# Kernel tuning notes

Measured on AMD Instinct MI355X. Metric: run time of the kernel, lower is better.

Reference implementation:

```python
import jax, jax.numpy as jnp
import numpy as np

N = 4096  # seq len, used for cos/sin positional reweighting


def _non_neg(x):
    # exp(x) for x<0, x+1 for x>=0
    return jnp.where(x < 0, jnp.exp(x), x + 1.0)


def setup_inputs() -> dict:
    key = jax.random.key(0)
    kq, kk, kv = jax.random.split(key, 3)
    shape = (4, 16, N, 64)
    q = jax.random.normal(kq, shape, dtype=jnp.float32)
    k = jax.random.normal(kk, shape, dtype=jnp.float32)
    v = jax.random.normal(kv, shape, dtype=jnp.float32)
    return {"q": q, "k": k, "v": v}


def reference(q, k, v):
    s = q.shape[-2]
    pos = (jnp.pi / 2.0 / s) * jnp.arange(s, dtype=q.dtype)
    cos = jnp.cos(pos)[:, None]  # [S, 1], broadcasts over feature dim
    sin = jnp.sin(pos)[:, None]
    qf = _non_neg(q)
    kf = _non_neg(k)
    q_cos, q_sin = qf * cos, qf * sin  # [B, H, S, D]
    k_cos, k_sin = kf * cos, kf * sin
    # O(N) kv aggregation: [B, H, D, Dv]
    kv_cos = jnp.einsum('bhsd,bhse->bhde', k_cos, v)
    kv_sin = jnp.einsum('bhsd,bhse->bhde', k_sin, v)
    out = jnp.einsum('bhsd,bhde->bhse', q_cos, kv_cos) + \
          jnp.einsum('bhsd,bhde->bhse', q_sin, kv_sin)
    return out
```

## Files before the change

### kernel.cpp

```cpp
#include <hip/hip_runtime.h>
#include <math.h>

#define SLEN 4096
#define DH   64
#define BHN  64
#define CH   8
#define ROWSPER 512
#define SPAD 72

typedef float  f32x4  __attribute__((ext_vector_type(4)));
typedef __bf16 bf16x8 __attribute__((ext_vector_type(8)));

static constexpr float ANG = 1.5707963267948966f / 4096.0f;

static __device__ __forceinline__ float featf(float x) {
    return x < 0.f ? __expf(x) : x + 1.f;
}
static __device__ __forceinline__ void pack2(short* p, float a, float b) {
    union { __bf16 h[2]; unsigned u; } uu;
    uu.h[0] = (__bf16)a; uu.h[1] = (__bf16)b;
    *(unsigned*)p = uu.u;
}

__global__ __launch_bounds__(256) void kv_partial(const float* __restrict__ k,
                                                  const float* __restrict__ v,
                                                  float* __restrict__ part)
{
    __shared__ short kcT[64 * SPAD];
    __shared__ short ksT[64 * SPAD];
    __shared__ short vT [64 * SPAD];

    const int bx = blockIdx.x;
    const int bh = bx >> 3, ch = bx & 7;
    const size_t base = (size_t)bh * SLEN * DH;
    const int t  = threadIdx.x;
    const int wv = t >> 6;
    const int ln = t & 63;
    const int m  = ln & 15;
    const int g  = ln >> 4;

    const int d0 = (t & 15) * 4;
    const int sg = t >> 4;

    f32x4 aC[4] = {}; f32x4 aS[4] = {};

    for (int tile = 0; tile < 8; ++tile) {
        const int srow0 = ch * ROWSPER + tile * 64;
        __syncthreads();
        #pragma unroll
        for (int it = 0; it < 2; ++it) {
            const int sl = it * 32 + sg * 2;
            const int srow = srow0 + sl;
            float sn0, c0, sn1, c1;
            __sincosf(ANG * (float)srow,       &sn0, &c0);
            __sincosf(ANG * (float)(srow + 1), &sn1, &c1);
            const f32x4 k0 = *(const f32x4*)&k[base + (size_t)srow * DH + d0];
            const f32x4 k1 = *(const f32x4*)&k[base + (size_t)(srow + 1) * DH + d0];
            const f32x4 v0 = *(const f32x4*)&v[base + (size_t)srow * DH + d0];
            const f32x4 v1 = *(const f32x4*)&v[base + (size_t)(srow + 1) * DH + d0];
            #pragma unroll
            for (int i = 0; i < 4; ++i) {
                const float kf0 = featf(k0[i]);
                const float kf1 = featf(k1[i]);
                const int rowoff = (d0 + i) * SPAD + sl;
                pack2(&kcT[rowoff], kf0 * c0,  kf1 * c1);
                pack2(&ksT[rowoff], kf0 * sn0, kf1 * sn1);
                pack2(&vT [rowoff], v0[i],     v1[i]);
            }
        }
        __syncthreads();
        #pragma unroll
        for (int b = 0; b < 2; ++b) {
            const int so = b * 32 + g * 8;
            const bf16x8 Ac = *(const bf16x8*)&kcT[(wv * 16 + m) * SPAD + so];
            const bf16x8 As = *(const bf16x8*)&ksT[(wv * 16 + m) * SPAD + so];
            #pragma unroll
            for (int nt = 0; nt < 4; ++nt) {
                const bf16x8 Bv = *(const bf16x8*)&vT[(nt * 16 + m) * SPAD + so];
                aC[nt] = __builtin_amdgcn_mfma_f32_16x16x32_bf16(Ac, Bv, aC[nt], 0, 0, 0);
                aS[nt] = __builtin_amdgcn_mfma_f32_16x16x32_bf16(As, Bv, aS[nt], 0, 0, 0);
            }
        }
    }

    const size_t pb = (size_t)bx * 8192;
    #pragma unroll
    for (int nt = 0; nt < 4; ++nt) {
        #pragma unroll
        for (int r = 0; r < 4; ++r) {
            const size_t rowb = (size_t)(wv * 16 + g * 4 + r) * 64 + nt * 16 + m;
            part[pb        + rowb] = aC[nt][r];
            part[pb + 4096 + rowb] = aS[nt][r];
        }
    }
}

__global__ __launch_bounds__(256) void kv_reduce(const float* __restrict__ part,
                                                 short* __restrict__ kvT)
{
    const int bx = blockIdx.x;
    const int bh = bx >> 2, qd = bx & 3;
    const size_t pbase = (size_t)bh * CH * 8192;
    for (int i = threadIdx.x; i < 2048; i += 256) {
        const int cs = i >> 10;
        const int dl = (i >> 6) & 15;
        const int e  = i & 63;
        const int d  = qd * 16 + dl;
        const int j  = cs * 4096 + d * 64 + e;
        float s = 0.f;
        #pragma unroll
        for (int c = 0; c < CH; ++c) s += part[pbase + (size_t)c * 8192 + j];
        __bf16 hv = (__bf16)s;
        kvT[(size_t)bh * 8192 + cs * 4096 + e * 64 + d] = *(short*)&hv;
    }
}

__global__ __launch_bounds__(256) void out_kernel(const float* __restrict__ q,
                                                  const short* __restrict__ kvT,
                                                  float* __restrict__ out)
{
    const int bx = blockIdx.x;
    const int bh = bx >> 4, chunk = bx & 15;
    const int t = threadIdx.x;
    const int wv = t >> 6, ln = t & 63, m = ln & 15, g = ln >> 4;
    const size_t qbase = (size_t)bh * SLEN * DH;
    const size_t kvb   = (size_t)bh * 8192;

    bf16x8 Bc[4][2], Bs[4][2];
    #pragma unroll
    for (int nt = 0; nt < 4; ++nt)
        #pragma unroll
        for (int b = 0; b < 2; ++b) {
            const int off = (nt * 16 + m) * 64 + b * 32 + g * 8;
            Bc[nt][b] = *(const bf16x8*)&kvT[kvb + off];
            Bs[nt][b] = *(const bf16x8*)&kvT[kvb + 4096 + off];
        }

    const int sA = chunk * 256 + wv * 16 + m;
    f32x4 qb[4], qn[4];
    #pragma unroll
    for (int p = 0; p < 4; ++p)
        qb[p] = *(const f32x4*)&q[qbase + (size_t)sA * DH + (p >> 1) * 32 + g * 8 + (p & 1) * 4];

    for (int it = 0; it < 4; ++it) {
        const int srow = sA + it * 64;
        if (it < 3) {
            #pragma unroll
            for (int p = 0; p < 4; ++p)
                qn[p] = *(const f32x4*)&q[qbase + (size_t)(srow + 64) * DH + (p >> 1) * 32 + g * 8 + (p & 1) * 4];
        }
        float sn, c;
        __sincosf(ANG * (float)srow, &sn, &c);
        union { bf16x8 v; __bf16 e[8]; } Ac[2], As[2];
        #pragma unroll
        for (int p = 0; p < 4; ++p) {
            #pragma unroll
            for (int i = 0; i < 4; ++i) {
                const float qf = featf(qb[p][i]);
                Ac[p >> 1].e[(p & 1) * 4 + i] = (__bf16)(qf * c);
                As[p >> 1].e[(p & 1) * 4 + i] = (__bf16)(qf * sn);
            }
        }
        f32x4 acc[4] = {};
        #pragma unroll
        for (int nt = 0; nt < 4; ++nt) {
            acc[nt] = __builtin_amdgcn_mfma_f32_16x16x32_bf16(Ac[0].v, Bc[nt][0], acc[nt], 0, 0, 0);
            acc[nt] = __builtin_amdgcn_mfma_f32_16x16x32_bf16(Ac[1].v, Bc[nt][1], acc[nt], 0, 0, 0);
            acc[nt] = __builtin_amdgcn_mfma_f32_16x16x32_bf16(As[0].v, Bs[nt][0], acc[nt], 0, 0, 0);
            acc[nt] = __builtin_amdgcn_mfma_f32_16x16x32_bf16(As[1].v, Bs[nt][1], acc[nt], 0, 0, 0);
        }
        const int s0 = chunk * 256 + (it * 4 + wv) * 16;
        #pragma unroll
        for (int r = 0; r < 4; ++r) {
            const size_t ob = ((size_t)bh * SLEN + s0 + g * 4 + r) * 64;
            #pragma unroll
            for (int nt = 0; nt < 4; ++nt)
                out[ob + nt * 16 + m] = acc[nt][r];
        }
        if (it < 3) {
            #pragma unroll
            for (int p = 0; p < 4; ++p) qb[p] = qn[p];
        }
    }
}

extern "C" void kernel_launch(void* const* d_in, const int* in_sizes, int n_in,
                              void* d_out, int out_size, void* d_ws, size_t ws_size,
                              hipStream_t stream) {
    const float* q = (const float*)d_in[0];
    const float* k = (const float*)d_in[1];
    const float* v = (const float*)d_in[2];
    float* out  = (float*)d_out;
    float* part = (float*)d_ws;
    short* kvT  = (short*)((char*)d_ws + (size_t)BHN * CH * 8192 * 4);

    hipLaunchKernelGGL(kv_partial, dim3(BHN * CH), dim3(256), 0, stream, k, v, part);
    hipLaunchKernelGGL(kv_reduce,  dim3(BHN * 4),  dim3(256), 0, stream, part, kvT);
    hipLaunchKernelGGL(out_kernel, dim3(BHN * 16), dim3(256), 0, stream, q, kvT, out);
}
```

Measured before the change: 74.40 us.

## Pipeline kv_partial loads, swizzle LDS, rotate sincos, store bf16 partials

kv_partial now splits each sequence into 16 chunks of 256 rows instead of 8 of 512. It double-buffers the global K/V loads in registers so the next tile's loads overlap the MFMA work. Per-row sincos calls are replaced by a single initial sincos followed by angle-addition rotations, and the LDS tiles use an XOR swizzle to cut bank conflicts. Partial sums are stored as bf16, and the reduce kernel reads them with vectorised loads over more blocks. This lowers workspace traffic and occupancy limits, at the cost of extra rounding from bf16 partials and small drift from the rotation recurrence.

```diff
diff --git a/kernel.cpp b/kernel.cpp
--- a/kernel.cpp
+++ b/kernel.cpp
@@ -4,14 +4,20 @@
 #define SLEN 4096
 #define DH   64
 #define BHN  64
-#define CH   8
-#define ROWSPER 512
+#define CH   16
+#define ROWSPER 256
+#define NT   4
 #define SPAD 72
 
 typedef float  f32x4  __attribute__((ext_vector_type(4)));
+typedef short  s16x4  __attribute__((ext_vector_type(4)));
 typedef __bf16 bf16x8 __attribute__((ext_vector_type(8)));
 
-static constexpr float ANG = 1.5707963267948966f / 4096.0f;
+static constexpr float ANG  = 1.5707963267948966f / 4096.0f;
+static constexpr float C1   = 0.9999999264657180f;
+static constexpr float S1   = 3.8349518757139556e-4f;
+static constexpr float ROTC = 0.9996988186962042f;
+static constexpr float ROTS = 0.024541228522912288f;
 
 static __device__ __forceinline__ float featf(float x) {
     return x < 0.f ? __expf(x) : x + 1.f;
@@ -21,98 +27,138 @@
     uu.h[0] = (__bf16)a; uu.h[1] = (__bf16)b;
     *(unsigned*)p = uu.u;
 }
+static __device__ __forceinline__ float b2f(short s) {
+    unsigned u = ((unsigned)(unsigned short)s) << 16;
+    float f; __builtin_memcpy(&f, &u, 4); return f;
+}
+static __device__ __forceinline__ short f2b(float f) {
+    __bf16 h = (__bf16)f; short s; __builtin_memcpy(&s, &h, 2); return s;
+}
 
 __global__ __launch_bounds__(256) void kv_partial(const float* __restrict__ k,
                                                   const float* __restrict__ v,
-                                                  float* __restrict__ part)
+                                                  short* __restrict__ part)
 {
     __shared__ short kcT[64 * SPAD];
     __shared__ short ksT[64 * SPAD];
     __shared__ short vT [64 * SPAD];
 
     const int bx = blockIdx.x;
-    const int bh = bx >> 3, ch = bx & 7;
+    const int bh = bx >> 4, ch = bx & 15;
     const size_t base = (size_t)bh * SLEN * DH;
     const int t  = threadIdx.x;
     const int wv = t >> 6;
     const int ln = t & 63;
     const int m  = ln & 15;
     const int g  = ln >> 4;
-
     const int d0 = (t & 15) * 4;
     const int sg = t >> 4;
+    const int srow_base = ch * ROWSPER;
+
+    float cA[2], sA[2], cB[2], sB[2];
+    #pragma unroll
+    for (int it = 0; it < 2; ++it) {
+        float sn, cs;
+        __sincosf(ANG * (float)(srow_base + it * 32 + sg * 2), &sn, &cs);
+        cA[it] = cs;            sA[it] = sn;
+        cB[it] = cs * C1 - sn * S1;
+        sB[it] = sn * C1 + cs * S1;
+    }
 
     f32x4 aC[4] = {}; f32x4 aS[4] = {};
-
-    for (int tile = 0; tile < 8; ++tile) {
-        const int srow0 = ch * ROWSPER + tile * 64;
-        __syncthreads();
+    f32x4 K0[2][2], K1[2][2], V0[2][2], V1[2][2];
+
+#define LOADT(BUF, TILE)                                                      \
+    _Pragma("unroll")                                                         \
+    for (int it = 0; it < 2; ++it) {                                          \
+        const size_t r = base + (size_t)(srow_base + (TILE) * 64 + it * 32 + sg * 2) * DH + d0; \
+        K0[BUF][it] = *(const f32x4*)&k[r];                                   \
+        K1[BUF][it] = *(const f32x4*)&k[r + DH];                              \
+        V0[BUF][it] = *(const f32x4*)&v[r];                                   \
+        V1[BUF][it] = *(const f32x4*)&v[r + DH];                              \
+    }
+
+    LOADT(0, 0);
+
+    #pragma unroll
+    for (int tile = 0; tile < NT; ++tile) {
+        const int buf = tile & 1;
+        if (tile) __syncthreads();
         #pragma unroll
         for (int it = 0; it < 2; ++it) {
             const int sl = it * 32 + sg * 2;
-            const int srow = srow0 + sl;
-            float sn0, c0, sn1, c1;
-            __sincosf(ANG * (float)srow,       &sn0, &c0);
-            __sincosf(ANG * (float)(srow + 1), &sn1, &c1);
-            const f32x4 k0 = *(const f32x4*)&k[base + (size_t)srow * DH + d0];
-            const f32x4 k1 = *(const f32x4*)&k[base + (size_t)(srow + 1) * DH + d0];
-            const f32x4 v0 = *(const f32x4*)&v[base + (size_t)srow * DH + d0];
-            const f32x4 v1 = *(const f32x4*)&v[base + (size_t)(srow + 1) * DH + d0];
             #pragma unroll
             for (int i = 0; i < 4; ++i) {
-                const float kf0 = featf(k0[i]);
-                const float kf1 = featf(k1[i]);
-                const int rowoff = (d0 + i) * SPAD + sl;
-                pack2(&kcT[rowoff], kf0 * c0,  kf1 * c1);
-                pack2(&ksT[rowoff], kf0 * sn0, kf1 * sn1);
-                pack2(&vT [rowoff], v0[i],     v1[i]);
+                const int d  = d0 + i;
+                const float kf0 = featf(K0[buf][it][i]);
+                const float kf1 = featf(K1[buf][it][i]);
+                const int pos = ((((sl >> 3) ^ ((d >> 2) & 7)) << 3) | (sl & 7));
+                const int ro  = d * SPAD + pos;
+                pack2(&kcT[ro], kf0 * cA[it], kf1 * cB[it]);
+                pack2(&ksT[ro], kf0 * sA[it], kf1 * sB[it]);
+                pack2(&vT [ro], V0[buf][it][i], V1[buf][it][i]);
             }
         }
         __syncthreads();
+        if (tile + 1 < NT) { LOADT(buf ^ 1, tile + 1); }
+        #pragma unroll
+        for (int it = 0; it < 2; ++it) {
+            float c = cA[it], s = sA[it];
+            cA[it] = c * ROTC - s * ROTS; sA[it] = s * ROTC + c * ROTS;
+            c = cB[it]; s = sB[it];
+            cB[it] = c * ROTC - s * ROTS; sB[it] = s * ROTC + c * ROTS;
+        }
         #pragma unroll
         for (int b = 0; b < 2; ++b) {
-            const int so = b * 32 + g * 8;
-            const bf16x8 Ac = *(const bf16x8*)&kcT[(wv * 16 + m) * SPAD + so];
-            const bf16x8 As = *(const bf16x8*)&ksT[(wv * 16 + m) * SPAD + so];
+            const int s3 = b * 4 + g;
+            const int dA = wv * 16 + m;
+            const int oA = dA * SPAD + ((s3 ^ ((dA >> 2) & 7)) << 3);
+            const bf16x8 Ac = *(const bf16x8*)&kcT[oA];
+            const bf16x8 As = *(const bf16x8*)&ksT[oA];
             #pragma unroll
             for (int nt = 0; nt < 4; ++nt) {
-                const bf16x8 Bv = *(const bf16x8*)&vT[(nt * 16 + m) * SPAD + so];
+                const int dB = nt * 16 + m;
+                const int oB = dB * SPAD + ((s3 ^ ((dB >> 2) & 7)) << 3);
+                const bf16x8 Bv = *(const bf16x8*)&vT[oB];
                 aC[nt] = __builtin_amdgcn_mfma_f32_16x16x32_bf16(Ac, Bv, aC[nt], 0, 0, 0);
                 aS[nt] = __builtin_amdgcn_mfma_f32_16x16x32_bf16(As, Bv, aS[nt], 0, 0, 0);
             }
         }
     }
+#undef LOADT
 
     const size_t pb = (size_t)bx * 8192;
     #pragma unroll
     for (int nt = 0; nt < 4; ++nt) {
         #pragma unroll
         for (int r = 0; r < 4; ++r) {
-            const size_t rowb = (size_t)(wv * 16 + g * 4 + r) * 64 + nt * 16 + m;
-            part[pb        + rowb] = aC[nt][r];
-            part[pb + 4096 + rowb] = aS[nt][r];
-        }
-    }
-}
-
-__global__ __launch_bounds__(256) void kv_reduce(const float* __restrict__ part,
+            const int rowb = (wv * 16 + g * 4 + r) * 64 + nt * 16 + m;
+            part[pb        + rowb] = f2b(aC[nt][r]);
+            part[pb + 4096 + rowb] = f2b(aS[nt][r]);
+        }
+    }
+}
+
+__global__ __launch_bounds__(256) void kv_reduce(const short* __restrict__ part,
                                                  short* __restrict__ kvT)
 {
     const int bx = blockIdx.x;
-    const int bh = bx >> 2, qd = bx & 3;
+    const int bh = bx >> 3, seg = bx & 7;
     const size_t pbase = (size_t)bh * CH * 8192;
-    for (int i = threadIdx.x; i < 2048; i += 256) {
-        const int cs = i >> 10;
-        const int dl = (i >> 6) & 15;
-        const int e  = i & 63;
-        const int d  = qd * 16 + dl;
-        const int j  = cs * 4096 + d * 64 + e;
-        float s = 0.f;
-        #pragma unroll
-        for (int c = 0; c < CH; ++c) s += part[pbase + (size_t)c * 8192 + j];
-        __bf16 hv = (__bf16)s;
-        kvT[(size_t)bh * 8192 + cs * 4096 + e * 64 + d] = *(short*)&hv;
-    }
+    const int j0 = seg * 1024 + threadIdx.x * 4;
+    float acc[4] = {};
+    #pragma unroll
+    for (int c = 0; c < CH; ++c) {
+        const s16x4 sv = *(const s16x4*)&part[pbase + (size_t)c * 8192 + j0];
+        #pragma unroll
+        for (int i = 0; i < 4; ++i) acc[i] += b2f(sv[i]);
+    }
+    const int cs = j0 >> 12;
+    const int d  = (j0 >> 6) & 63;
+    const int e0 = j0 & 63;
+    #pragma unroll
+    for (int i = 0; i < 4; ++i)
+        kvT[(size_t)bh * 8192 + cs * 4096 + (e0 + i) * 64 + d] = f2b(acc[i]);
 }
 
 __global__ __launch_bounds__(256) void out_kernel(const float* __restrict__ q,
@@ -191,10 +237,10 @@
     const float* k = (const float*)d_in[1];
     const float* v = (const float*)d_in[2];
     float* out  = (float*)d_out;
-    float* part = (float*)d_ws;
-    short* kvT  = (short*)((char*)d_ws + (size_t)BHN * CH * 8192 * 4);
+    short* part = (short*)d_ws;
+    short* kvT  = (short*)((char*)d_ws + (size_t)BHN * CH * 8192 * 2);
 
     hipLaunchKernelGGL(kv_partial, dim3(BHN * CH), dim3(256), 0, stream, k, v, part);
-    hipLaunchKernelGGL(kv_reduce,  dim3(BHN * 4),  dim3(256), 0, stream, part, kvT);
+    hipLaunchKernelGGL(kv_reduce,  dim3(BHN * 8),  dim3(256), 0, stream, part, kvT);
     hipLaunchKernelGGL(out_kernel, dim3(BHN * 16), dim3(256), 0, stream, q, kvT, out);
 }
```

New measurement: 66.83 us. -10.2%, faster.
